# Optimization experiments

Measured on AMD Instinct MI355X. Metric: run time of the kernel, lower is better.

## Reference

```python
import jax, jax.numpy as jnp
import numpy as np

NF = 64      # feature channels of h
K = 3        # dynamic filter spatial size (padding=1 in source implies k=3)
FACTOR = 4   # pixel-unshuffle factor


def shuffle_down(x, f):
    # torch pixel_unshuffle: (B,C,H*f,W*f) -> (B,C*f*f,H,W)
    B, C, H, W = x.shape
    x = x.reshape(B, C, H // f, f, W // f, f)
    x = x.transpose(0, 1, 3, 5, 2, 4)
    return x.reshape(B, C * f * f, H // f, W // f)


def _patches3x3(x):
    # x: (B,C,H,W) -> (B,C,9,H,W): zero-padded 3x3 neighborhoods, row-major taps,
    # identical to the identity-filter grouped conv (im2col) in the source.
    H, W = x.shape[-2], x.shape[-1]
    xp = jnp.pad(x, ((0, 0), (0, 0), (1, 1), (1, 1)))
    shifts = [xp[:, :, dy:dy + H, dx:dx + W] for dy in range(K) for dx in range(K)]
    return jnp.stack(shifts, axis=2)


def setup_inputs() -> dict:
    key = jax.random.key(0)
    k1, k2, k3, k4 = jax.random.split(key, 4)
    B, H, W = 2, 256, 256
    h = jax.random.normal(k1, (B, NF, H, W), dtype=jnp.float32)
    i_t = jax.random.normal(k2, (B, 3, H * FACTOR, W * FACTOR), dtype=jnp.float32)
    conv_w = jax.random.normal(k3, (K * K, 3 * FACTOR ** 2, K, K), dtype=jnp.float32) * 0.05
    conv_b = jax.random.normal(k4, (K * K,), dtype=jnp.float32) * 0.05
    return {"h": h, "i_t": i_t, "conv_w": conv_w, "conv_b": conv_b}


def reference(h, i_t, conv_w, conv_b):
    # predict per-pixel 3x3 filters from the shuffled-down guidance frame
    x = shuffle_down(i_t, FACTOR)  # (B, 48, H, W)
    f = jax.lax.conv_general_dilated(
        x, conv_w, window_strides=(1, 1), padding=((1, 1), (1, 1)),
        dimension_numbers=("NCHW", "OIHW", "NCHW"))
    filters = jax.nn.relu(f + conv_b[None, :, None, None])  # (B, 9, H, W)

    # dynamic per-pixel conv: same 3x3 filter applied to every channel of h
    patches = _patches3x3(h)  # (B, nf, 9, H, W)
    out = jnp.einsum("bcfhw,bfhw->bchw", patches, filters)  # (B, nf, H, W)
    return out
```

## Files before the change

### kernel.cpp

```cpp
#include <hip/hip_runtime.h>

#define TILE 16
#define HSZ 256
#define WSZ 256
#define NFC 64
#define PLANE (HSZ * WSZ)

typedef __attribute__((ext_vector_type(8))) short short8;
typedef __attribute__((ext_vector_type(4))) float f32x4;

__device__ inline unsigned short f2bf(float f) {
    unsigned u = __builtin_bit_cast(unsigned, f);
    return (unsigned short)((u + 0x7fffu + ((u >> 16) & 1u)) >> 16);
}

__global__ void prep_wfrag(const float* __restrict__ wbuf,
                           unsigned short* __restrict__ wfragG)
{
    const int kb   = blockIdx.x;
    const int lane = threadIdx.x;
    const int l15  = lane & 15;
    const int kg   = lane >> 4;
    unsigned short v8[8];
#pragma unroll
    for (int j = 0; j < 8; ++j) {
        const int k = kb * 32 + kg * 8 + j;
        float w = 0.f;
        if (k < 432 && l15 < 9) {
            const int kk = k / 48;
            const int ic = k - kk * 48;
            w = wbuf[l15 * 432 + ic * 9 + kk];
        }
        v8[j] = f2bf(w);
    }
    unsigned short* p = wfragG + (size_t)kb * 512 + lane * 8;
    *(ushort4*)(p)     = ushort4{v8[0], v8[1], v8[2], v8[3]};
    *(ushort4*)(p + 4) = ushort4{v8[4], v8[5], v8[6], v8[7]};
}

__global__ __launch_bounds__(128) void filter_conv_mfma2(
    const float* __restrict__ i_t,
    const unsigned short* __restrict__ wfragG,
    const float* __restrict__ bias,
    float* __restrict__ fbuf)
{
    __shared__ __align__(16) unsigned short xs[180 * 48];

    const int tid  = threadIdx.x;
    const int X0 = blockIdx.x * 16;
    const int Y0 = blockIdx.y * 8;
    const int b  = blockIdx.z;
    const int lane = tid & 63;
    const int l15  = tid & 15;
    const int kg   = (tid >> 4) & 3;
    const int wv   = tid >> 6;

    const float bv = (l15 < 9) ? bias[l15] : 0.f;
    const float* itb = i_t + (size_t)b * 3 * (PLANE * 16);

    {
        ushort4 sreg[9]; int sdst[9];
#pragma unroll
        for (int k = 0; k < 9; ++k) {
            const int v = tid + 128 * k;
            const int sp = v / 12, t = v - sp * 12;
            const int c3 = t >> 2, fy = t & 3;
            const int ly = sp / 18, lx = sp - ly * 18;
            const int Y = Y0 - 1 + ly, X = X0 - 1 + lx;
            float4 val = make_float4(0.f, 0.f, 0.f, 0.f);
            if ((unsigned)Y < HSZ && (unsigned)X < WSZ)
                val = *(const float4*)(itb + ((size_t)c3 * 1024 + (4 * Y + fy)) * 1024 + 4 * X);
            sreg[k] = ushort4{f2bf(val.x), f2bf(val.y), f2bf(val.z), f2bf(val.w)};
            sdst[k] = sp * 48 + t * 4;
        }
#pragma unroll
        for (int k = 0; k < 9; ++k) *(ushort4*)(xs + sdst[k]) = sreg[k];
    }
    {
        ushort4 sreg[8]; int sdst[8];
#pragma unroll
        for (int k = 0; k < 8; ++k) {
            const int v = tid + 128 * (k + 9);
            const int sp = v / 12, t = v - sp * 12;
            const int c3 = t >> 2, fy = t & 3;
            const int ly = sp / 18, lx = sp - ly * 18;
            const int Y = Y0 - 1 + ly, X = X0 - 1 + lx;
            float4 val = make_float4(0.f, 0.f, 0.f, 0.f);
            if (v < 2160 && (unsigned)Y < HSZ && (unsigned)X < WSZ)
                val = *(const float4*)(itb + ((size_t)c3 * 1024 + (4 * Y + fy)) * 1024 + 4 * X);
            sreg[k] = ushort4{f2bf(val.x), f2bf(val.y), f2bf(val.z), f2bf(val.w)};
            sdst[k] = (v < 2160) ? (sp * 48 + t * 4) : -1;
        }
#pragma unroll
        for (int k = 0; k < 8; ++k)
            if (sdst[k] >= 0) *(ushort4*)(xs + sdst[k]) = sreg[k];
    }

    short8 wf[14];
#pragma unroll
    for (int kb = 0; kb < 14; ++kb)
        wf[kb] = *(const short8*)(wfragG + (size_t)kb * 512 + lane * 8);

    __syncthreads();

    f32x4 acc0 = {0.f, 0.f, 0.f, 0.f}, acc1 = acc0, acc2 = acc0, acc3 = acc0;
#pragma unroll
    for (int kb = 0; kb < 14; ++kb) {
        const int k0 = kb * 32 + kg * 8;
        int off = 0;
        if (k0 < 432) {
            const int kk  = k0 / 48;
            const int ic0 = k0 - kk * 48;
            const int ky  = kk / 3;
            const int kx  = kk - 3 * ky;
            off = ((wv * 4 + ky) * 18 + l15 + kx) * 48 + ic0;
        }
        short8 a0 = *(const short8*)(xs + off);
        short8 a1 = *(const short8*)(xs + off + 864);
        short8 a2 = *(const short8*)(xs + off + 1728);
        short8 a3 = *(const short8*)(xs + off + 2592);
        acc0 = __builtin_amdgcn_mfma_f32_16x16x32_bf16(a0, wf[kb], acc0, 0, 0, 0);
        acc1 = __builtin_amdgcn_mfma_f32_16x16x32_bf16(a1, wf[kb], acc1, 0, 0, 0);
        acc2 = __builtin_amdgcn_mfma_f32_16x16x32_bf16(a2, wf[kb], acc2, 0, 0, 0);
        acc3 = __builtin_amdgcn_mfma_f32_16x16x32_bf16(a3, wf[kb], acc3, 0, 0, 0);
    }

    __syncthreads();
    float* lf = (float*)xs;
    if (l15 < 9) {
#pragma unroll
        for (int i = 0; i < 4; ++i) {
            const int py = wv * 4 + i;
            f32x4 A = (i == 0) ? acc0 : (i == 1) ? acc1 : (i == 2) ? acc2 : acc3;
#pragma unroll
            for (int r = 0; r < 4; ++r) {
                const int px = kg * 4 + r;
                lf[(py * 16 + px) * 12 + l15] = fmaxf(A[r] + bv, 0.f);
            }
        }
    }
    __syncthreads();
    float* fb = fbuf + (size_t)b * PLANE * 12;
#pragma unroll
    for (int k = 0; k < 3; ++k) {
        const int v = tid + 128 * k;
        const int row = v / 48, off = v - row * 48;
        *(float4*)(fb + ((size_t)(Y0 + row) * WSZ + X0) * 12 + off * 4) =
            *(const float4*)(lf + v * 4);
    }
}

__global__ __launch_bounds__(256) void dyn_apply3(
    const float* __restrict__ hbuf,
    const float* __restrict__ fbuf,
    float* __restrict__ out)
{
    __shared__ __align__(16) float hs[8 * 432];

    const int tid  = threadIdx.x;
    const int pxq  = tid & 3;
    const int py   = (tid >> 2) & 15;
    const int c_lo = tid >> 6;
    const int cg = blockIdx.x & 7;
    const int X0 = (blockIdx.x >> 3) * TILE;
    const int Y0 = blockIdx.y * TILE;
    const int b  = blockIdx.z;

    float flt[4][9];
    {
        const float* fb = fbuf + ((size_t)b * PLANE + (size_t)(Y0 + py) * WSZ + X0 + pxq * 4) * 12;
#pragma unroll
        for (int j = 0; j < 4; ++j) {
            float4 f0 = *(const float4*)(fb + j * 12);
            float4 f1 = *(const float4*)(fb + j * 12 + 4);
            float  f8 = fb[j * 12 + 8];
            flt[j][0] = f0.x; flt[j][1] = f0.y; flt[j][2] = f0.z; flt[j][3] = f0.w;
            flt[j][4] = f1.x; flt[j][5] = f1.y; flt[j][6] = f1.z; flt[j][7] = f1.w;
            flt[j][8] = f8;
        }
    }

    const float* hp = hbuf + ((size_t)b * NFC + cg * 8) * PLANE;
    {
        float4 rv[4]; int vv[4];
#pragma unroll
        for (int k = 0; k < 4; ++k) {
            const int v = tid + 256 * k;
            vv[k] = v;
            const int c = v / 108, r = v - c * 108;
            const int row = r / 6, xf4 = r - row * 6;
            const int Y  = Y0 - 1 + row;
            const int X4 = X0 - 4 + xf4 * 4;
            float4 val = make_float4(0.f, 0.f, 0.f, 0.f);
            if (v < 864 && (unsigned)Y < HSZ && (unsigned)X4 < WSZ)
                val = *(const float4*)(hp + (size_t)c * PLANE + (size_t)Y * WSZ + X4);
            rv[k] = val;
        }
#pragma unroll
        for (int k = 0; k < 4; ++k)
            if (vv[k] < 864) *(float4*)(hs + vv[k] * 4) = rv[k];
    }
    __syncthreads();

    float a[2][4];
#pragma unroll
    for (int cc = 0; cc < 2; ++cc)
#pragma unroll
        for (int j = 0; j < 4; ++j) a[cc][j] = 0.f;

#pragma unroll
    for (int cc = 0; cc < 2; ++cc) {
        const float* pl = hs + (c_lo + 4 * cc) * 432;
#pragma unroll
        for (int ky = 0; ky < 3; ++ky) {
            const float* rp = pl + (py + ky) * 24 + pxq * 4;
            float4 w0 = *(const float4*)rp;
            float4 w1 = *(const float4*)(rp + 4);
            float  w8 = rp[8];
            const float vs[9] = {w0.x, w0.y, w0.z, w0.w, w1.x, w1.y, w1.z, w1.w, w8};
#pragma unroll
            for (int kx = 0; kx < 3; ++kx)
#pragma unroll
                for (int j = 0; j < 4; ++j)
                    a[cc][j] = fmaf(vs[3 + kx + j], flt[j][ky * 3 + kx], a[cc][j]);
        }
    }

#pragma unroll
    for (int cc = 0; cc < 2; ++cc) {
        const int ch = cg * 8 + c_lo + 4 * cc;
        *(float4*)(out + ((size_t)b * NFC + ch) * PLANE
                       + (size_t)(Y0 + py) * WSZ + X0 + pxq * 4)
            = make_float4(a[cc][0], a[cc][1], a[cc][2], a[cc][3]);
    }
}

__global__ void filter_conv_mfma(const float* __restrict__ i_t,
                                 const float* __restrict__ wbuf,
                                 const float* __restrict__ bias,
                                 float* __restrict__ fbuf)
{
    __shared__ __align__(16) unsigned short xs[324 * 56];

    const int tid = threadIdx.x;
    const int X0 = blockIdx.x * TILE;
    const int Y0 = blockIdx.y * TILE;
    const int b  = blockIdx.z;
    const int l15 = tid & 15;
    const int kg  = (tid >> 4) & 3;
    const int wv  = tid >> 6;

    float* wsh = (float*)xs;
    for (int i = tid; i < 3888; i += 256) wsh[i] = wbuf[i];
    __syncthreads();

    short8 wfrag[14];
#pragma unroll
    for (int kb = 0; kb < 14; ++kb) {
#pragma unroll
        for (int j = 0; j < 8; ++j) {
            const int k = kb * 32 + kg * 8 + j;
            float w = 0.f;
            if (k < 432 && l15 < 9) {
                const int kk = k / 48;
                const int ic = k - kk * 48;
                w = wsh[l15 * 432 + ic * 9 + kk];
            }
            wfrag[kb][j] = (short)f2bf(w);
        }
    }
    const float bv = (l15 < 9) ? bias[l15] : 0.f;
    __syncthreads();

    const float* itb = i_t + (size_t)b * 3 * (PLANE * 16);
    for (int v = tid; v < 3888; v += 256) {
        const int sp = v / 12;
        const int t  = v - sp * 12;
        const int c3 = t >> 2, fy = t & 3;
        const int ly = sp / 18, lx = sp - ly * 18;
        const int Y = Y0 - 1 + ly, X = X0 - 1 + lx;
        float4 val = make_float4(0.f, 0.f, 0.f, 0.f);
        if (Y >= 0 && Y < HSZ && X >= 0 && X < WSZ)
            val = *(const float4*)(itb + ((size_t)c3 * 1024 + (4 * Y + fy)) * 1024 + 4 * X);
        ushort4 u;
        u.x = f2bf(val.x); u.y = f2bf(val.y); u.z = f2bf(val.z); u.w = f2bf(val.w);
        *(ushort4*)(xs + sp * 56 + t * 4) = u;
    }
    __syncthreads();

    f32x4 acc0 = {0.f, 0.f, 0.f, 0.f}, acc1 = acc0, acc2 = acc0, acc3 = acc0;
#pragma unroll
    for (int kb = 0; kb < 14; ++kb) {
        const int k0 = kb * 32 + kg * 8;
        int off = 0;
        if (k0 < 432) {
            const int kk  = k0 / 48;
            const int ic0 = k0 - kk * 48;
            const int ky  = kk / 3;
            const int kx  = kk - 3 * ky;
            off = ((wv * 4 + ky) * 18 + l15 + kx) * 56 + ic0;
        }
        short8 a0 = *(const short8*)(xs + off);
        short8 a1 = *(const short8*)(xs + off + 1008);
        short8 a2 = *(const short8*)(xs + off + 2016);
        short8 a3 = *(const short8*)(xs + off + 3024);
        acc0 = __builtin_amdgcn_mfma_f32_16x16x32_bf16(a0, wfrag[kb], acc0, 0, 0, 0);
        acc1 = __builtin_amdgcn_mfma_f32_16x16x32_bf16(a1, wfrag[kb], acc1, 0, 0, 0);
        acc2 = __builtin_amdgcn_mfma_f32_16x16x32_bf16(a2, wfrag[kb], acc2, 0, 0, 0);
        acc3 = __builtin_amdgcn_mfma_f32_16x16x32_bf16(a3, wfrag[kb], acc3, 0, 0, 0);
    }

    if (l15 < 9) {
        float* fb = fbuf + (size_t)b * PLANE * 12;
#pragma unroll
        for (int i = 0; i < 4; ++i) {
            const int py = wv * 4 + i;
            f32x4 A = (i == 0) ? acc0 : (i == 1) ? acc1 : (i == 2) ? acc2 : acc3;
#pragma unroll
            for (int r = 0; r < 4; ++r) {
                const int px = kg * 4 + r;
                fb[((size_t)(Y0 + py) * WSZ + X0 + px) * 12 + l15] = fmaxf(A[r] + bv, 0.f);
            }
        }
    }
}

__global__ __launch_bounds__(256, 2) void fused_dynfilter(
    const float* __restrict__ hbuf,
    const float* __restrict__ i_t,
    const float* __restrict__ wbuf,
    const float* __restrict__ bias,
    float* __restrict__ out)
{
    __shared__ __align__(16) float smem[15552];
    float4* xs4 = (float4*)smem;

    const int tid = threadIdx.x;
    const int px = tid & 15;
    const int py = tid >> 4;
    const int X0 = blockIdx.x * TILE;
    const int Y0 = blockIdx.y * TILE;
    const int b  = blockIdx.z;

    const float* itb = i_t + (size_t)b * 3 * 1024 * 1024;
    for (int v = tid; v < 3888; v += 256) {
        int sp = v / 12;
        int t  = v - sp * 12;
        int c3 = t >> 2, fy = t & 3;
        int ly = sp / 18, lx = sp - ly * 18;
        int Y = Y0 - 1 + ly, X = X0 - 1 + lx;
        float4 val = make_float4(0.f, 0.f, 0.f, 0.f);
        if (Y >= 0 && Y < HSZ && X >= 0 && X < WSZ)
            val = *(const float4*)(itb + ((size_t)c3 * 1024 + (4 * Y + fy)) * 1024 + 4 * X);
        xs4[t * 324 + sp] = val;
    }
    __syncthreads();

    float acc[9];
#pragma unroll
    for (int oc = 0; oc < 9; ++oc) acc[oc] = bias[oc];

#pragma unroll 1
    for (int ky = 0; ky < 3; ++ky)
#pragma unroll 1
        for (int kx = 0; kx < 3; ++kx) {
            const int sp = (py + ky) * 18 + (px + kx);
            const int kk = ky * 3 + kx;
#pragma unroll
            for (int ic4 = 0; ic4 < 12; ++ic4) {
                float4 v = xs4[ic4 * 324 + sp];
                const int chb = ((ic4 >> 2) << 4) + ((ic4 & 3) << 2);
                const float* wp = wbuf + (size_t)chb * 9 + kk;
                const float vv[4] = {v.x, v.y, v.z, v.w};
#pragma unroll
                for (int j = 0; j < 4; ++j)
#pragma unroll
                    for (int oc = 0; oc < 9; ++oc)
                        acc[oc] = fmaf(vv[j], wp[j * 9 + (size_t)oc * 432], acc[oc]);
            }
        }

    float flt[9];
#pragma unroll
    for (int oc = 0; oc < 9; ++oc) flt[oc] = fmaxf(acc[oc], 0.f);

    float4* hs4 = (float4*)smem;
#pragma unroll 1
    for (int cg = 0; cg < 16; ++cg) {
        __syncthreads();
        const float* hp = hbuf + ((size_t)b * NFC + cg * 4) * PLANE;
        for (int idx = tid; idx < 1296; idx += 256) {
            int c  = idx / 324;
            int sp = idx - c * 324;
            int ly = sp / 18, lx = sp - ly * 18;
            int Y = Y0 - 1 + ly, X = X0 - 1 + lx;
            float vv = 0.f;
            if (Y >= 0 && Y < HSZ && X >= 0 && X < WSZ)
                vv = hp[(size_t)c * PLANE + (size_t)Y * WSZ + X];
            smem[sp * 4 + c] = vv;
        }
        __syncthreads();

        float s0 = 0.f, s1 = 0.f, s2 = 0.f, s3 = 0.f;
#pragma unroll
        for (int ky = 0; ky < 3; ++ky)
#pragma unroll
            for (int kx = 0; kx < 3; ++kx) {
                float4 v = hs4[(py + ky) * 18 + (px + kx)];
                float f = flt[ky * 3 + kx];
                s0 = fmaf(v.x, f, s0);
                s1 = fmaf(v.y, f, s1);
                s2 = fmaf(v.z, f, s2);
                s3 = fmaf(v.w, f, s3);
            }
        size_t o = (((size_t)b * NFC + cg * 4) * HSZ + (Y0 + py)) * WSZ + (X0 + px);
        out[o]                     = s0;
        out[o + (size_t)PLANE]     = s1;
        out[o + (size_t)2 * PLANE] = s2;
        out[o + (size_t)3 * PLANE] = s3;
    }
}

extern "C" void kernel_launch(void* const* d_in, const int* in_sizes, int n_in,
                              void* d_out, int out_size, void* d_ws, size_t ws_size,
                              hipStream_t stream) {
    const float* h      = (const float*)d_in[0];
    const float* i_t    = (const float*)d_in[1];
    const float* conv_w = (const float*)d_in[2];
    const float* conv_b = (const float*)d_in[3];
    float* out = (float*)d_out;

    const int B = in_sizes[0] / (NFC * PLANE);
    const size_t fbuf_sz  = (size_t)B * PLANE * 12 * sizeof(float);
    const size_t wfrag_sz = 14 * 512 * sizeof(unsigned short);

    if (ws_size >= fbuf_sz + wfrag_sz) {
        float* fbuf = (float*)d_ws;
        unsigned short* wfragG = (unsigned short*)((char*)d_ws + fbuf_sz);
        prep_wfrag<<<dim3(14), 64, 0, stream>>>(conv_w, wfragG);
        dim3 g1(WSZ / 16, HSZ / 8, B);
        filter_conv_mfma2<<<g1, 128, 0, stream>>>(i_t, wfragG, conv_b, fbuf);
        dim3 g2((WSZ / TILE) * 8, HSZ / TILE, B);
        dyn_apply3<<<g2, 256, 0, stream>>>(h, fbuf, out);
    } else if (ws_size >= fbuf_sz) {
        float* fbuf = (float*)d_ws;
        dim3 g1(WSZ / TILE, HSZ / TILE, B);
        filter_conv_mfma<<<g1, 256, 0, stream>>>(i_t, conv_w, conv_b, fbuf);
        dim3 g2((WSZ / TILE) * 8, HSZ / TILE, B);
        dyn_apply3<<<g2, 256, 0, stream>>>(h, fbuf, out);
    } else {
        dim3 grid(WSZ / TILE, HSZ / TILE, B);
        fused_dynfilter<<<grid, 256, 0, stream>>>(h, i_t, conv_w, conv_b, out);
    }
}
```

Baseline: 138.7 us.

## Widen dyn_apply tile to 32 columns and batch all filter-conv loads before stores

The dynamic-filter apply kernel now covers 32 columns per block instead of 16. Each thread computes 4 channels instead of 2, so the per-pixel filter taps loaded from the filter buffer are reused across more channels. Halo loading switches from float4 to scalar loads with a padded shared-memory row stride of 40, and launch bounds request 4 blocks per CU. In the filter conv kernel, all 17 input loads are issued before any bf16 conversion or shared store to raise memory-level parallelism, at the cost of more live registers.

```diff
diff --git a/kernel.cpp b/kernel.cpp
--- a/kernel.cpp
+++ b/kernel.cpp
@@ -59,28 +59,10 @@
     const float* itb = i_t + (size_t)b * 3 * (PLANE * 16);
 
     {
-        ushort4 sreg[9]; int sdst[9];
-#pragma unroll
-        for (int k = 0; k < 9; ++k) {
+        float4 lreg[17]; int sdst[17];
+#pragma unroll
+        for (int k = 0; k < 17; ++k) {
             const int v = tid + 128 * k;
-            const int sp = v / 12, t = v - sp * 12;
-            const int c3 = t >> 2, fy = t & 3;
-            const int ly = sp / 18, lx = sp - ly * 18;
-            const int Y = Y0 - 1 + ly, X = X0 - 1 + lx;
-            float4 val = make_float4(0.f, 0.f, 0.f, 0.f);
-            if ((unsigned)Y < HSZ && (unsigned)X < WSZ)
-                val = *(const float4*)(itb + ((size_t)c3 * 1024 + (4 * Y + fy)) * 1024 + 4 * X);
-            sreg[k] = ushort4{f2bf(val.x), f2bf(val.y), f2bf(val.z), f2bf(val.w)};
-            sdst[k] = sp * 48 + t * 4;
-        }
-#pragma unroll
-        for (int k = 0; k < 9; ++k) *(ushort4*)(xs + sdst[k]) = sreg[k];
-    }
-    {
-        ushort4 sreg[8]; int sdst[8];
-#pragma unroll
-        for (int k = 0; k < 8; ++k) {
-            const int v = tid + 128 * (k + 9);
             const int sp = v / 12, t = v - sp * 12;
             const int c3 = t >> 2, fy = t & 3;
             const int ly = sp / 18, lx = sp - ly * 18;
@@ -88,12 +70,16 @@
             float4 val = make_float4(0.f, 0.f, 0.f, 0.f);
             if (v < 2160 && (unsigned)Y < HSZ && (unsigned)X < WSZ)
                 val = *(const float4*)(itb + ((size_t)c3 * 1024 + (4 * Y + fy)) * 1024 + 4 * X);
-            sreg[k] = ushort4{f2bf(val.x), f2bf(val.y), f2bf(val.z), f2bf(val.w)};
+            lreg[k] = val;
             sdst[k] = (v < 2160) ? (sp * 48 + t * 4) : -1;
         }
 #pragma unroll
-        for (int k = 0; k < 8; ++k)
-            if (sdst[k] >= 0) *(ushort4*)(xs + sdst[k]) = sreg[k];
+        for (int k = 0; k < 17; ++k) {
+            if (sdst[k] >= 0) {
+                ushort4 u{f2bf(lreg[k].x), f2bf(lreg[k].y), f2bf(lreg[k].z), f2bf(lreg[k].w)};
+                *(ushort4*)(xs + sdst[k]) = u;
+            }
+        }
     }
 
     short8 wf[14];
@@ -150,25 +136,25 @@
     }
 }
 
-__global__ __launch_bounds__(256) void dyn_apply3(
+__global__ __launch_bounds__(256, 4) void dyn_apply4(
     const float* __restrict__ hbuf,
     const float* __restrict__ fbuf,
     float* __restrict__ out)
 {
-    __shared__ __align__(16) float hs[8 * 432];
+    __shared__ __align__(16) float hs[8 * 18 * 40];
 
     const int tid  = threadIdx.x;
-    const int pxq  = tid & 3;
-    const int py   = (tid >> 2) & 15;
-    const int c_lo = tid >> 6;
+    const int pq   = tid & 7;
+    const int py   = (tid >> 3) & 15;
+    const int c_lo = tid >> 7;
     const int cg = blockIdx.x & 7;
-    const int X0 = (blockIdx.x >> 3) * TILE;
+    const int X0 = (blockIdx.x >> 3) * 32;
     const int Y0 = blockIdx.y * TILE;
     const int b  = blockIdx.z;
 
     float flt[4][9];
     {
-        const float* fb = fbuf + ((size_t)b * PLANE + (size_t)(Y0 + py) * WSZ + X0 + pxq * 4) * 12;
+        const float* fb = fbuf + ((size_t)b * PLANE + (size_t)(Y0 + py) * WSZ + X0 + pq * 4) * 12;
 #pragma unroll
         for (int j = 0; j < 4; ++j) {
             float4 f0 = *(const float4*)(fb + j * 12);
@@ -182,38 +168,39 @@
 
     const float* hp = hbuf + ((size_t)b * NFC + cg * 8) * PLANE;
     {
-        float4 rv[4]; int vv[4];
-#pragma unroll
-        for (int k = 0; k < 4; ++k) {
+        float rv[20]; int dst[20];
+#pragma unroll
+        for (int k = 0; k < 20; ++k) {
             const int v = tid + 256 * k;
-            vv[k] = v;
-            const int c = v / 108, r = v - c * 108;
-            const int row = r / 6, xf4 = r - row * 6;
-            const int Y  = Y0 - 1 + row;
-            const int X4 = X0 - 4 + xf4 * 4;
-            float4 val = make_float4(0.f, 0.f, 0.f, 0.f);
-            if (v < 864 && (unsigned)Y < HSZ && (unsigned)X4 < WSZ)
-                val = *(const float4*)(hp + (size_t)c * PLANE + (size_t)Y * WSZ + X4);
+            const int c = v / 612;
+            const int r = v - c * 612;
+            const int row = r / 34, l = r - row * 34;
+            const int Y = Y0 - 1 + row;
+            const int X = X0 - 1 + l;
+            float val = 0.f;
+            if (v < 4896 && (unsigned)Y < HSZ && (unsigned)X < WSZ)
+                val = hp[(size_t)c * PLANE + (size_t)Y * WSZ + X];
             rv[k] = val;
-        }
-#pragma unroll
-        for (int k = 0; k < 4; ++k)
-            if (vv[k] < 864) *(float4*)(hs + vv[k] * 4) = rv[k];
-    }
-    __syncthreads();
-
-    float a[2][4];
-#pragma unroll
-    for (int cc = 0; cc < 2; ++cc)
+            dst[k] = (v < 4896) ? (c * 720 + row * 40 + 3 + l) : -1;
+        }
+#pragma unroll
+        for (int k = 0; k < 20; ++k)
+            if (dst[k] >= 0) hs[dst[k]] = rv[k];
+    }
+    __syncthreads();
+
+    float a[4][4];
+#pragma unroll
+    for (int cc = 0; cc < 4; ++cc)
 #pragma unroll
         for (int j = 0; j < 4; ++j) a[cc][j] = 0.f;
 
 #pragma unroll
-    for (int cc = 0; cc < 2; ++cc) {
-        const float* pl = hs + (c_lo + 4 * cc) * 432;
+    for (int cc = 0; cc < 4; ++cc) {
+        const float* pl = hs + (c_lo + 2 * cc) * 720;
 #pragma unroll
         for (int ky = 0; ky < 3; ++ky) {
-            const float* rp = pl + (py + ky) * 24 + pxq * 4;
+            const float* rp = pl + (py + ky) * 40 + pq * 4;
             float4 w0 = *(const float4*)rp;
             float4 w1 = *(const float4*)(rp + 4);
             float  w8 = rp[8];
@@ -227,10 +214,10 @@
     }
 
 #pragma unroll
-    for (int cc = 0; cc < 2; ++cc) {
-        const int ch = cg * 8 + c_lo + 4 * cc;
+    for (int cc = 0; cc < 4; ++cc) {
+        const int ch = cg * 8 + c_lo + 2 * cc;
         *(float4*)(out + ((size_t)b * NFC + ch) * PLANE
-                       + (size_t)(Y0 + py) * WSZ + X0 + pxq * 4)
+                       + (size_t)(Y0 + py) * WSZ + X0 + pq * 4)
             = make_float4(a[cc][0], a[cc][1], a[cc][2], a[cc][3]);
     }
 }
@@ -440,14 +427,14 @@
         prep_wfrag<<<dim3(14), 64, 0, stream>>>(conv_w, wfragG);
         dim3 g1(WSZ / 16, HSZ / 8, B);
         filter_conv_mfma2<<<g1, 128, 0, stream>>>(i_t, wfragG, conv_b, fbuf);
-        dim3 g2((WSZ / TILE) * 8, HSZ / TILE, B);
-        dyn_apply3<<<g2, 256, 0, stream>>>(h, fbuf, out);
+        dim3 g2((WSZ / 32) * 8, HSZ / TILE, B);
+        dyn_apply4<<<g2, 256, 0, stream>>>(h, fbuf, out);
     } else if (ws_size >= fbuf_sz) {
         float* fbuf = (float*)d_ws;
         dim3 g1(WSZ / TILE, HSZ / TILE, B);
         filter_conv_mfma<<<g1, 256, 0, stream>>>(i_t, conv_w, conv_b, fbuf);
-        dim3 g2((WSZ / TILE) * 8, HSZ / TILE, B);
-        dyn_apply3<<<g2, 256, 0, stream>>>(h, fbuf, out);
+        dim3 g2((WSZ / 32) * 8, HSZ / TILE, B);
+        dyn_apply4<<<g2, 256, 0, stream>>>(h, fbuf, out);
     } else {
         dim3 grid(WSZ / TILE, HSZ / TILE, B);
         fused_dynfilter<<<grid, 256, 0, stream>>>(h, i_t, conv_w, conv_b, out);
```

New measurement: 137.7 us. Within noise of the previous version (-0.7%).
